# Kernel optimization log

Measured on AMD Instinct MI355X. Metric: run time of the kernel, lower is better.

The kernel has to match this reference:

```python
import jax, jax.numpy as jnp
import numpy as np

NUM_TYPES = 8
NUM_TAGS = 1 + 2 * NUM_TYPES  # tag 0 = 'O', 2t+1 = 'B-t', 2t+2 = 'I-t'
NEG = -10000.0


def _bio_constraints(num_types):
    K = 1 + 2 * num_types
    allowed = np.zeros((K, K), dtype=np.float32)
    for i in range(K):
        for j in range(K):
            if j == 0 or (j % 2 == 1):  # to O or to B-y: always allowed
                allowed[i, j] = 1.0
            else:  # to I-y: only from B-y or I-y
                y = (j - 2) // 2
                if i in (2 * y + 1, 2 * y + 2):
                    allowed[i, j] = 1.0
    start = np.array([1.0 if (j == 0 or j % 2 == 1) else 0.0 for j in range(K)], dtype=np.float32)
    end = np.ones((K,), dtype=np.float32)  # BIO: any tag may end a sequence
    return allowed, start, end


def setup_inputs() -> dict:
    key = jax.random.key(0)
    ks = jax.random.split(key, 8)
    B, T, D, K = 64, 512, 1024, NUM_TAGS
    mlm_out = jax.random.normal(ks[0], (B, T, D), dtype=jnp.float32)
    lengths = jax.random.randint(ks[1], (B,), T // 4, T + 1)  # variable lengths >= 1
    mask = (jnp.arange(T)[None, :] < lengths[:, None])  # bool [B,T], left-padded-free
    gold = jax.random.randint(ks[2], (B, T), 0, K)
    W = jax.random.normal(ks[3], (D, K), dtype=jnp.float32) * 0.02
    b = jnp.zeros((K,), dtype=jnp.float32)
    transitions = jax.random.normal(ks[4], (K, K), dtype=jnp.float32) * 0.1
    start_trans = jax.random.normal(ks[5], (K,), dtype=jnp.float32) * 0.1
    end_trans = jax.random.normal(ks[6], (K,), dtype=jnp.float32) * 0.1
    ta, sa, ea = _bio_constraints(NUM_TYPES)
    return {"mlm_out": mlm_out, "mask": mask, "gold": gold, "W": W, "b": b,
            "transitions": transitions, "start_trans": start_trans, "end_trans": end_trans,
            "trans_allowed": jnp.asarray(ta), "start_allowed": jnp.asarray(sa), "end_allowed": jnp.asarray(ea)}


def reference(mlm_out, mask, gold, W, b, transitions, start_trans, end_trans,
              trans_allowed, start_allowed, end_allowed):
    logits = jnp.einsum('btd,dk->btk', mlm_out, W) + b  # [B,T,K]
    maskf = mask.astype(logits.dtype)
    B, T, K = logits.shape

    # ---- joint (numerator) score, AllenNLP semantics ----
    score = start_trans[gold[:, 0]]
    pair = transitions[gold[:, :-1], gold[:, 1:]]                       # [B,T-1]
    emit = jnp.take_along_axis(logits, gold[:, :, None], axis=2)[..., 0]  # [B,T]
    score = score + jnp.sum(pair * maskf[:, 1:], axis=1) + jnp.sum(emit[:, :-1] * maskf[:, :-1], axis=1)
    lengths = jnp.sum(mask.astype(jnp.int32), axis=1)
    last_tags = jnp.take_along_axis(gold, (lengths - 1)[:, None], axis=1)[:, 0]
    last_emit = jnp.take_along_axis(logits[:, -1, :], last_tags[:, None], axis=1)[:, 0]
    score = score + end_trans[last_tags] + last_emit * maskf[:, -1]

    # ---- partition function (forward algorithm, log-space scan over time) ----
    logits_t = jnp.swapaxes(logits, 0, 1)  # [T,B,K]
    mask_t = jnp.swapaxes(maskf, 0, 1)     # [T,B]
    alpha0 = start_trans + logits_t[0]

    def fstep(alpha, xs):
        emit_t, m = xs
        inner = alpha[:, :, None] + transitions[None] + emit_t[:, None, :]  # [B,K,K]
        new = jax.scipy.special.logsumexp(inner, axis=1)
        return jnp.where(m[:, None] > 0, new, alpha), None

    alphaT, _ = jax.lax.scan(fstep, alpha0, (logits_t[1:], mask_t[1:]))
    logZ = jax.scipy.special.logsumexp(alphaT + end_trans, axis=1)

    loss = -jnp.sum(score - logZ)  # loss_weight = 1.0

    # ---- Viterbi decode with BIO-constrained transitions ----
    ct = transitions * trans_allowed + NEG * (1.0 - trans_allowed)
    cs = start_trans * start_allowed + NEG * (1.0 - start_allowed)
    ce = end_trans * end_allowed + NEG * (1.0 - end_allowed)
    v0 = cs + logits_t[0]

    def vstep(v, xs):
        emit_t, m = xs
        inner = v[:, :, None] + ct[None]          # [B,K,K]
        bp = jnp.argmax(inner, axis=1)            # [B,K] best prev tag per next tag
        best = jnp.max(inner, axis=1) + emit_t
        return jnp.where(m[:, None] > 0, best, v), bp

    vT, bps = jax.lax.scan(vstep, v0, (logits_t[1:], mask_t[1:]))  # bps [T-1,B,K]
    last_tag = jnp.argmax(vT + ce, axis=1)  # [B]

    def btstep(tag, xs):
        bp, m = xs
        prev = jnp.take_along_axis(bp, tag[:, None], axis=1)[:, 0]
        prev = jnp.where(m > 0, prev, tag)  # padded steps: carry tag through
        return prev, tag

    first_tag, tags_rest = jax.lax.scan(btstep, last_tag, (bps, mask_t[1:]), reverse=True)
    pred = jnp.concatenate([first_tag[None], tags_rest], axis=0).swapaxes(0, 1)  # [B,T]
    pred = pred * mask.astype(pred.dtype)
    return logits, loss, pred
```

## Files before the change

kernel.cpp:

```cpp
#include <hip/hip_runtime.h>
#include <math.h>

#define KK 17
#define TT 512
#define DD 1024
#define NBATCH 64
#define NEGC -10000.0f
#define NINF -1e30f

__device__ __forceinline__ float wsum64(float v) {
#pragma unroll
  for (int s = 32; s >= 1; s >>= 1) v += __shfl_xor(v, s);
  return v;
}
__device__ __forceinline__ float wmax64(float v) {
#pragma unroll
  for (int s = 32; s >= 1; s >>= 1) v = fmaxf(v, __shfl_xor(v, s));
  return v;
}
__device__ __forceinline__ int wsum64i(int v) {
#pragma unroll
  for (int s = 32; s >= 1; s >>= 1) v += __shfl_xor(v, s);
  return v;
}

__global__ __launch_bounds__(512) void k_logits(const float* __restrict__ X,
                                                const float* __restrict__ W,
                                                const float* __restrict__ b,
                                                float* __restrict__ logits) {
  __shared__ float Ws[512 * KK];
  const int tid = threadIdx.x;
  const int lane = tid & 63;
  const int wv = tid >> 6;
  const long r0 = (long)blockIdx.x * 16 + wv * 2;
  const float* x0 = X + r0 * DD;
  float a0[KK], a1[KK];
#pragma unroll
  for (int j = 0; j < KK; ++j) { a0[j] = 0.f; a1[j] = 0.f; }

  for (int half = 0; half < 2; ++half) {
    __syncthreads();
#pragma unroll
    for (int i = 0; i < KK; ++i) {
      int idx = tid + i * 512;
      Ws[idx] = W[half * 512 * KK + idx];
    }
    __syncthreads();
#pragma unroll
    for (int it = 0; it < 8; ++it) {
      int k = it * 64 + lane;
      float xa = x0[half * 512 + k];
      float xb = x0[DD + half * 512 + k];
#pragma unroll
      for (int j = 0; j < KK; ++j) {
        float w = Ws[k * KK + j];
        a0[j] = fmaf(xa, w, a0[j]);
        a1[j] = fmaf(xb, w, a1[j]);
      }
    }
  }
#pragma unroll
  for (int j = 0; j < KK; ++j) { a0[j] = wsum64(a0[j]); a1[j] = wsum64(a1[j]); }
  if (lane < KK) {
    float v0 = 0.f, v1 = 0.f;
#pragma unroll
    for (int j = 0; j < KK; ++j)
      if (lane == j) { v0 = a0[j]; v1 = a1[j]; }
    float bb = b[lane];
    logits[r0 * KK + lane] = v0 + bb;
    logits[(r0 + 1) * KK + lane] = v1 + bb;
  }
}

__global__ __launch_bounds__(128) void k_scan(
    const float* __restrict__ logits, const void* __restrict__ maskp,
    const int* __restrict__ gold, const float* __restrict__ trans,
    const float* __restrict__ st, const float* __restrict__ et,
    const float* __restrict__ ta, const float* __restrict__ sa,
    const float* __restrict__ ea, float* __restrict__ lossp,
    float* __restrict__ predp) {
  __shared__ __align__(16) float EM[513 * KK];
  __shared__ __align__(4) unsigned char Mk[512];
  __shared__ unsigned char BPt[511 * KK];
  __shared__ unsigned char G2t[256 * KK];
  __shared__ unsigned char G4t[128 * KK];
  __shared__ unsigned char G8t[64 * KK];
  __shared__ unsigned char PR[512];
  __shared__ float red[2];
  __shared__ int slen[2];
  __shared__ int shlt;

  const int tid = threadIdx.x;
  const int lane = tid & 63;
  const int wv = tid >> 6;
  const int batch = blockIdx.x & 63;
  const int role = blockIdx.x >> 6;
  const float* Lg = logits + (size_t)batch * TT * KK;

  const unsigned char* mb = (const unsigned char*)maskp;
  const bool m_is_i32 = (mb[1] == 0);

  {
    const float4* Lg4 = reinterpret_cast<const float4*>(Lg);
    float4* EM4 = reinterpret_cast<float4*>(EM);
    for (int i = tid; i < (TT * KK) / 4; i += 128) {
      float4 v = Lg4[i];
      if (role == 0) {
        v.x = expf(v.x); v.y = expf(v.y); v.z = expf(v.z); v.w = expf(v.w);
      }
      EM4[i] = v;
    }
    if (m_is_i32) {
      const int* mi = (const int*)maskp + batch * TT;
      for (int t2 = tid; t2 < TT; t2 += 128) Mk[t2] = (unsigned char)(mi[t2] != 0);
    } else {
      const unsigned char* mB = mb + batch * TT;
      for (int t2 = tid; t2 < TT; t2 += 128) Mk[t2] = (unsigned char)(mB[t2] != 0);
    }
  }
  __syncthreads();
  {
    unsigned int m4 = *reinterpret_cast<const unsigned int*>(&Mk[tid * 4]);
    int c = (int)((m4 * 0x01010101u) >> 24);
    c = wsum64i(c);
    if (lane == 0) slen[wv] = c;
  }
  __syncthreads();
  const int len = slen[0] + slen[1];

  if (role == 0) {
    if (wv == 0) {
      const int jc = lane < KK ? lane : (KK - 1);
      const bool act = lane < KK;
      float Pcol[KK];
#pragma unroll
      for (int i = 0; i < KK; ++i) Pcol[i] = expf(trans[i * KK + jc]);
      float a0 = st[jc] + Lg[jc];
      float m0 = wmax64(act ? a0 : NINF);
      float qown = expf(a0 - m0);
      float C = m0;
      float q[KK];
#pragma unroll
      for (int i = 0; i < KK; ++i) q[i] = __shfl(qown, i);
      float ee = EM[KK + jc];
      for (int t = 1; t < len; ++t) {
        float ee_n = EM[(t + 1) * KK + jc];
        float da = fmaf(q[0], Pcol[0], fmaf(q[4], Pcol[4], fmaf(q[8], Pcol[8], fmaf(q[12], Pcol[12], q[16] * Pcol[16]))));
        float db = fmaf(q[1], Pcol[1], fmaf(q[5], Pcol[5], fmaf(q[9], Pcol[9], q[13] * Pcol[13])));
        float dc = fmaf(q[2], Pcol[2], fmaf(q[6], Pcol[6], fmaf(q[10], Pcol[10], q[14] * Pcol[14])));
        float dd = fmaf(q[3], Pcol[3], fmaf(q[7], Pcol[7], fmaf(q[11], Pcol[11], q[15] * Pcol[15])));
        float qn = ((da + db) + (dc + dd)) * ee;
        ee = ee_n;
#pragma unroll
        for (int i = 0; i < KK; ++i) q[i] = __shfl(qn, i);
        qown = qn;
        if ((t & 7) == 0) {
          float s0 = ((q[0] + q[1]) + (q[2] + q[3])) + ((q[4] + q[5]) + (q[6] + q[7]));
          float s1 = ((q[8] + q[9]) + (q[10] + q[11])) + ((q[12] + q[13]) + (q[14] + q[15]));
          float s = (s0 + s1) + q[16];
          float inv = 1.0f / s;
          C += logf(s);
#pragma unroll
          for (int i = 0; i < KK; ++i) q[i] *= inv;
          qown *= inv;
        }
      }
      float term = act ? qown * expf(et[jc]) : 0.f;
      float S = wsum64(term);
      if (lane == 0) red[0] = C + logf(S);
    } else {
      const int* gb = gold + batch * TT;
      float esum = 0.f, tsum = 0.f;
#pragma unroll
      for (int u = 0; u < 8; ++u) {
        int t = lane + 64 * u;
        int gt = gb[t];
        float mt = (float)Mk[t];
        esum += mt * Lg[t * KK + gt];
        int tn = (t + 1 < TT) ? t + 1 : TT - 1;
        int gn = gb[tn];
        float mtr = (t + 1 < TT && Mk[t + 1]) ? 1.f : 0.f;
        tsum += mtr * trans[gt * KK + gn];
      }
      float ssum = wsum64(esum + tsum);
      if (lane == 0) red[1] = ssum + st[gb[0]] + et[gb[len - 1]];
    }
    __syncthreads();
    if (tid == 0) atomicAdd(lossp, red[0] - red[1]);
  } else {
    if (wv == 0) {
      const int jj = lane & 31;
      const int h = lane >> 5;
      const int jc = jj < KK ? jj : (KK - 1);
      const int i0 = h ? 9 : 0;
      const int ni = h ? 8 : 9;
      float ctv[9];
#pragma unroll
      for (int r = 0; r < 9; ++r) {
        int i = i0 + r;
        int ic = i < KK ? i : (KK - 1);
        float cv = (ta[ic * KK + jc] > 0.5f) ? trans[ic * KK + jc] : NEGC;
        ctv[r] = (r < ni) ? cv : NINF;
      }
      float v = ((sa[jc] > 0.5f) ? st[jc] : NEGC) + EM[jc];
      float ec = EM[KK + jc];
      for (int t = 1; t < len; ++t) {
        float en = EM[(t + 1) * KK + jc];
        float c0 = __shfl(v, i0 + 0) + ctv[0];
        float c1 = __shfl(v, i0 + 1) + ctv[1];
        float c2 = __shfl(v, i0 + 2) + ctv[2];
        float c3 = __shfl(v, i0 + 3) + ctv[3];
        float c4 = __shfl(v, i0 + 4) + ctv[4];
        float c5 = __shfl(v, i0 + 5) + ctv[5];
        float c6 = __shfl(v, i0 + 6) + ctv[6];
        float c7 = __shfl(v, i0 + 7) + ctv[7];
        float c8 = __shfl(v, i0 + 8) + ctv[8];
        float v01 = c1 > c0 ? c1 : c0; int i01 = c1 > c0 ? i0 + 1 : i0;
        float v23 = c3 > c2 ? c3 : c2; int i23 = c3 > c2 ? i0 + 3 : i0 + 2;
        float v45 = c5 > c4 ? c5 : c4; int i45 = c5 > c4 ? i0 + 5 : i0 + 4;
        float v67 = c7 > c6 ? c7 : c6; int i67 = c7 > c6 ? i0 + 7 : i0 + 6;
        float v03 = v23 > v01 ? v23 : v01; int i03 = v23 > v01 ? i23 : i01;
        float v47 = v67 > v45 ? v67 : v45; int i47 = v67 > v45 ? i67 : i45;
        float v07 = v47 > v03 ? v47 : v03; int i07 = v47 > v03 ? i47 : i03;
        float bv = c8 > v07 ? c8 : v07;   int bi = c8 > v07 ? i0 + 8 : i07;
        float ov = __shfl_xor(bv, 32);
        int oi = __shfl_xor(bi, 32);
        bool take = (ov > bv) || (ov == bv && oi < bi);
        bv = take ? ov : bv;
        bi = take ? oi : bi;
        BPt[(t - 1) * KK + jc] = (unsigned char)bi;
        v = bv + ec;
        ec = en;
      }
      float fv = (jj < KK) ? (v + ((ea[jc] > 0.5f) ? et[jc] : NEGC)) : NINF;
      int fi = jc;
#pragma unroll
      for (int s = 32; s >= 1; s >>= 1) {
        float ov = __shfl_xor(fv, s); int oi = __shfl_xor(fi, s);
        bool take = (ov > fv) || (ov == fv && oi < fi);
        fv = take ? ov : fv; fi = take ? oi : fi;
      }
      if (tid == 0) shlt = fi;
    }
    __syncthreads();
    const int lt = shlt;
    for (int m = tid; m < 256; m += 128) {
      int s1 = 2 * m + 1, s0 = 2 * m;
      bool u1 = (s1 < 511) && Mk[s1 + 1];
      bool u0 = Mk[s0 + 1] != 0;
#pragma unroll
      for (int x = 0; x < KK; ++x) {
        int y = u1 ? (int)BPt[s1 * KK + x] : x;
        int z = u0 ? (int)BPt[s0 * KK + y] : y;
        G2t[m * KK + x] = (unsigned char)z;
      }
    }
    __syncthreads();
    {
      int p = tid;
#pragma unroll
      for (int x = 0; x < KK; ++x) {
        int y = G2t[(2 * p + 1) * KK + x];
        G4t[p * KK + x] = G2t[2 * p * KK + y];
      }
    }
    __syncthreads();
    if (tid < 64) {
      int p = tid;
#pragma unroll
      for (int x = 0; x < KK; ++x) {
        int y = G4t[(2 * p + 1) * KK + x];
        G8t[p * KK + x] = G4t[2 * p * KK + y];
      }
    }
    __syncthreads();
    if (tid == 0) {
      int x = lt;
      for (int p = 63; p >= 0; --p) {
        x = G8t[p * KK + x];
        PR[8 * p] = (unsigned char)x;
      }
    }
    __syncthreads();
    if (tid < 64) {
      int p = tid;
      int src = (p == 63) ? lt : (int)PR[8 * p + 8];
      PR[8 * p + 4] = G4t[(2 * p + 1) * KK + src];
    }
    __syncthreads();
    {
      int m = tid;
      int src = (m == 127) ? lt : (int)PR[4 * m + 4];
      PR[4 * m + 2] = G2t[(2 * m + 1) * KK + src];
    }
    __syncthreads();
    for (int m = tid; m < 256; m += 128) {
      int s = 2 * m + 1;
      int src = (m == 255) ? lt : (int)PR[2 * m + 2];
      int val = ((s < 511) && Mk[s + 1]) ? (int)BPt[s * KK + src] : src;
      PR[2 * m + 1] = (unsigned char)val;
    }
    __syncthreads();
    float* po = predp + batch * TT;
    for (int t2 = tid; t2 < TT; t2 += 128) po[t2] = Mk[t2] ? (float)PR[t2] : 0.f;
  }
}

extern "C" void kernel_launch(void* const* d_in, const int* in_sizes, int n_in,
                              void* d_out, int out_size, void* d_ws, size_t ws_size,
                              hipStream_t stream) {
  const float* mlm = (const float*)d_in[0];
  const void* mask = d_in[1];
  const int* gold = (const int*)d_in[2];
  const float* W = (const float*)d_in[3];
  const float* b = (const float*)d_in[4];
  const float* trans = (const float*)d_in[5];
  const float* st = (const float*)d_in[6];
  const float* et = (const float*)d_in[7];
  const float* ta = (const float*)d_in[8];
  const float* sa = (const float*)d_in[9];
  const float* ea = (const float*)d_in[10];

  float* out = (float*)d_out;
  float* logits = out;
  float* lossp = out + (size_t)NBATCH * TT * KK;
  float* predp = lossp + 1;

  hipMemsetAsync(lossp, 0, sizeof(float), stream);
  k_logits<<<dim3(2048), dim3(512), 0, stream>>>(mlm, W, b, logits);
  k_scan<<<dim3(128), dim3(128), 0, stream>>>(logits, mask, gold, trans, st, et,
                                              ta, sa, ea, lossp, predp);
}
```

Before: 365.8 us.

## Merge forward and Viterbi scans into one block per batch using readlane broadcasts

The scan kernel now runs one 256-thread block per batch instead of two 128-thread blocks with separate roles. Viterbi, the forward algorithm and the gold score run concurrently on different wavefronts of the same block, sharing one load of the logits into LDS. Cross-lane shuffles are replaced with readlane broadcasts, and the Viterbi loop uses all 17 candidates per lane instead of splitting them across two half-waves. Exp is moved into the forward loop using fast __expf/__logf intrinsics, which changes numerical precision slightly.

New measurement: 368.3 us. No clear change (+0.7%).

```diff
diff --git a/kernel.cpp b/kernel.cpp
--- a/kernel.cpp
+++ b/kernel.cpp
@@ -13,15 +13,13 @@
   for (int s = 32; s >= 1; s >>= 1) v += __shfl_xor(v, s);
   return v;
 }
-__device__ __forceinline__ float wmax64(float v) {
-#pragma unroll
-  for (int s = 32; s >= 1; s >>= 1) v = fmaxf(v, __shfl_xor(v, s));
-  return v;
-}
 __device__ __forceinline__ int wsum64i(int v) {
 #pragma unroll
   for (int s = 32; s >= 1; s >>= 1) v += __shfl_xor(v, s);
   return v;
+}
+__device__ __forceinline__ float rl(float x, int i) {
+  return __int_as_float(__builtin_amdgcn_readlane(__float_as_int(x), i));
 }
 
 __global__ __launch_bounds__(512) void k_logits(const float* __restrict__ X,
@@ -72,7 +70,10 @@
   }
 }
 
-__global__ __launch_bounds__(128) void k_scan(
+#define ARGM(vl, il, vr, ir, vo, io) \
+  { bool tk = (vr) > (vl); vo = tk ? (vr) : (vl); io = tk ? (ir) : (il); }
+
+__global__ __launch_bounds__(256) void k_scan(
     const float* __restrict__ logits, const void* __restrict__ maskp,
     const int* __restrict__ gold, const float* __restrict__ trans,
     const float* __restrict__ st, const float* __restrict__ et,
@@ -87,14 +88,12 @@
   __shared__ unsigned char G8t[64 * KK];
   __shared__ unsigned char PR[512];
   __shared__ float red[2];
-  __shared__ int slen[2];
   __shared__ int shlt;
 
   const int tid = threadIdx.x;
   const int lane = tid & 63;
   const int wv = tid >> 6;
-  const int batch = blockIdx.x & 63;
-  const int role = blockIdx.x >> 6;
+  const int batch = blockIdx.x;
   const float* Lg = logits + (size_t)batch * TT * KK;
 
   const unsigned char* mb = (const unsigned char*)maskp;
@@ -103,207 +102,201 @@
   {
     const float4* Lg4 = reinterpret_cast<const float4*>(Lg);
     float4* EM4 = reinterpret_cast<float4*>(EM);
-    for (int i = tid; i < (TT * KK) / 4; i += 128) {
-      float4 v = Lg4[i];
-      if (role == 0) {
-        v.x = expf(v.x); v.y = expf(v.y); v.z = expf(v.z); v.w = expf(v.w);
-      }
-      EM4[i] = v;
-    }
+    for (int i = tid; i < (TT * KK) / 4; i += 256) EM4[i] = Lg4[i];
     if (m_is_i32) {
       const int* mi = (const int*)maskp + batch * TT;
-      for (int t2 = tid; t2 < TT; t2 += 128) Mk[t2] = (unsigned char)(mi[t2] != 0);
+      for (int t2 = tid; t2 < TT; t2 += 256) Mk[t2] = (unsigned char)(mi[t2] != 0);
     } else {
       const unsigned char* mB = mb + batch * TT;
-      for (int t2 = tid; t2 < TT; t2 += 128) Mk[t2] = (unsigned char)(mB[t2] != 0);
-    }
-  }
-  __syncthreads();
+      for (int t2 = tid; t2 < TT; t2 += 256) Mk[t2] = (unsigned char)(mB[t2] != 0);
+    }
+  }
+  __syncthreads();
+  int len;
   {
-    unsigned int m4 = *reinterpret_cast<const unsigned int*>(&Mk[tid * 4]);
-    int c = (int)((m4 * 0x01010101u) >> 24);
-    c = wsum64i(c);
-    if (lane == 0) slen[wv] = c;
-  }
-  __syncthreads();
-  const int len = slen[0] + slen[1];
-
-  if (role == 0) {
-    if (wv == 0) {
-      const int jc = lane < KK ? lane : (KK - 1);
-      const bool act = lane < KK;
-      float Pcol[KK];
-#pragma unroll
-      for (int i = 0; i < KK; ++i) Pcol[i] = expf(trans[i * KK + jc]);
-      float a0 = st[jc] + Lg[jc];
-      float m0 = wmax64(act ? a0 : NINF);
-      float qown = expf(a0 - m0);
-      float C = m0;
-      float q[KK];
-#pragma unroll
-      for (int i = 0; i < KK; ++i) q[i] = __shfl(qown, i);
-      float ee = EM[KK + jc];
-      for (int t = 1; t < len; ++t) {
-        float ee_n = EM[(t + 1) * KK + jc];
-        float da = fmaf(q[0], Pcol[0], fmaf(q[4], Pcol[4], fmaf(q[8], Pcol[8], fmaf(q[12], Pcol[12], q[16] * Pcol[16]))));
-        float db = fmaf(q[1], Pcol[1], fmaf(q[5], Pcol[5], fmaf(q[9], Pcol[9], q[13] * Pcol[13])));
-        float dc = fmaf(q[2], Pcol[2], fmaf(q[6], Pcol[6], fmaf(q[10], Pcol[10], q[14] * Pcol[14])));
-        float dd = fmaf(q[3], Pcol[3], fmaf(q[7], Pcol[7], fmaf(q[11], Pcol[11], q[15] * Pcol[15])));
-        float qn = ((da + db) + (dc + dd)) * ee;
-        ee = ee_n;
-#pragma unroll
-        for (int i = 0; i < KK; ++i) q[i] = __shfl(qn, i);
-        qown = qn;
-        if ((t & 7) == 0) {
-          float s0 = ((q[0] + q[1]) + (q[2] + q[3])) + ((q[4] + q[5]) + (q[6] + q[7]));
-          float s1 = ((q[8] + q[9]) + (q[10] + q[11])) + ((q[12] + q[13]) + (q[14] + q[15]));
-          float s = (s0 + s1) + q[16];
-          float inv = 1.0f / s;
-          C += logf(s);
-#pragma unroll
-          for (int i = 0; i < KK; ++i) q[i] *= inv;
-          qown *= inv;
-        }
+    const unsigned int* Mku = reinterpret_cast<const unsigned int*>(Mk);
+    unsigned int a = Mku[lane], b2 = Mku[64 + lane];
+    int c = (int)(((a * 0x01010101u) >> 24) + ((b2 * 0x01010101u) >> 24));
+    len = wsum64i(c);
+  }
+
+  const int jc = lane < KK ? lane : (KK - 1);
+
+  if (wv == 0) {
+    float ctv[KK];
+#pragma unroll
+    for (int i = 0; i < KK; ++i)
+      ctv[i] = (ta[i * KK + jc] > 0.5f) ? trans[i * KK + jc] : NEGC;
+    float v = ((sa[jc] > 0.5f) ? st[jc] : NEGC) + EM[jc];
+    float ec = EM[KK + jc];
+    const float* EMp = EM + 2 * KK + jc;
+    unsigned char* bpw = BPt + jc;
+    const bool act = lane < KK;
+    for (int t = 1; t < len; ++t) {
+      float en = *EMp;
+      EMp += KK;
+      float c0 = rl(v, 0) + ctv[0],  c1 = rl(v, 1) + ctv[1];
+      float c2 = rl(v, 2) + ctv[2],  c3 = rl(v, 3) + ctv[3];
+      float c4 = rl(v, 4) + ctv[4],  c5 = rl(v, 5) + ctv[5];
+      float c6 = rl(v, 6) + ctv[6],  c7 = rl(v, 7) + ctv[7];
+      float c8 = rl(v, 8) + ctv[8],  c9 = rl(v, 9) + ctv[9];
+      float c10 = rl(v, 10) + ctv[10], c11 = rl(v, 11) + ctv[11];
+      float c12 = rl(v, 12) + ctv[12], c13 = rl(v, 13) + ctv[13];
+      float c14 = rl(v, 14) + ctv[14], c15 = rl(v, 15) + ctv[15];
+      float c16 = rl(v, 16) + ctv[16];
+      float d0, d1, d2, d3, d4, d5, d6, d7;
+      int j0, j1, j2, j3, j4, j5, j6, j7;
+      ARGM(c0, 0, c1, 1, d0, j0)     ARGM(c2, 2, c3, 3, d1, j1)
+      ARGM(c4, 4, c5, 5, d2, j2)     ARGM(c6, 6, c7, 7, d3, j3)
+      ARGM(c8, 8, c9, 9, d4, j4)     ARGM(c10, 10, c11, 11, d5, j5)
+      ARGM(c12, 12, c13, 13, d6, j6) ARGM(c14, 14, c15, 15, d7, j7)
+      float e0, e1, e2, e3; int k0, k1, k2, k3;
+      ARGM(d0, j0, d1, j1, e0, k0)   ARGM(d2, j2, d3, j3, e1, k1)
+      ARGM(d4, j4, d5, j5, e2, k2)   ARGM(d6, j6, d7, j7, e3, k3)
+      float f0, f1; int l0, l1;
+      ARGM(e0, k0, e1, k1, f0, l0)   ARGM(e2, k2, e3, k3, f1, l1)
+      float g0; int m0i;
+      ARGM(f0, l0, f1, l1, g0, m0i)
+      float bv; int bi;
+      ARGM(g0, m0i, c16, 16, bv, bi)
+      if (act) bpw[0] = (unsigned char)bi;
+      bpw += KK;
+      v = bv + ec;
+      ec = en;
+    }
+    float fv = v + ((ea[jc] > 0.5f) ? et[jc] : NEGC);
+    float best = rl(fv, 0);
+    int bidx = 0;
+#pragma unroll
+    for (int i = 1; i < KK; ++i) {
+      float fi = rl(fv, i);
+      bool tk = fi > best;
+      best = tk ? fi : best;
+      bidx = tk ? i : bidx;
+    }
+    if (tid == 0) shlt = bidx;
+  } else if (wv == 1) {
+    float Pcol[KK];
+#pragma unroll
+    for (int i = 0; i < KK; ++i) Pcol[i] = __expf(trans[i * KK + jc]);
+    float a0 = st[jc] + EM[jc];
+    float m0 = rl(a0, 0);
+#pragma unroll
+    for (int i = 1; i < KK; ++i) m0 = fmaxf(m0, rl(a0, i));
+    float qown = __expf(a0 - m0);
+    float C = m0;
+    float ee = __expf(EM[KK + jc]);
+    const float* EMp = EM + 2 * KK + jc;
+    for (int t = 1; t < len; ++t) {
+      float en_raw = *EMp;
+      EMp += KK;
+      float q0 = rl(qown, 0), q1 = rl(qown, 1), q2 = rl(qown, 2), q3 = rl(qown, 3);
+      float q4 = rl(qown, 4), q5 = rl(qown, 5), q6 = rl(qown, 6), q7 = rl(qown, 7);
+      float q8 = rl(qown, 8), q9 = rl(qown, 9), q10 = rl(qown, 10), q11 = rl(qown, 11);
+      float q12 = rl(qown, 12), q13 = rl(qown, 13), q14 = rl(qown, 14), q15 = rl(qown, 15);
+      float q16 = rl(qown, 16);
+      float da = fmaf(q0, Pcol[0], fmaf(q4, Pcol[4], fmaf(q8, Pcol[8], fmaf(q12, Pcol[12], q16 * Pcol[16]))));
+      float db = fmaf(q1, Pcol[1], fmaf(q5, Pcol[5], fmaf(q9, Pcol[9], q13 * Pcol[13])));
+      float dc = fmaf(q2, Pcol[2], fmaf(q6, Pcol[6], fmaf(q10, Pcol[10], q14 * Pcol[14])));
+      float dd = fmaf(q3, Pcol[3], fmaf(q7, Pcol[7], fmaf(q11, Pcol[11], q15 * Pcol[15])));
+      float qn = ((da + db) + (dc + dd)) * ee;
+      ee = __expf(en_raw);
+      if ((t & 7) == 0) {
+        float s0 = ((q0 + q1) + (q2 + q3)) + ((q4 + q5) + (q6 + q7));
+        float s1 = ((q8 + q9) + (q10 + q11)) + ((q12 + q13) + (q14 + q15));
+        float s = (s0 + s1) + q16;
+        C += __logf(s);
+        qn *= (1.0f / s);
       }
-      float term = act ? qown * expf(et[jc]) : 0.f;
-      float S = wsum64(term);
-      if (lane == 0) red[0] = C + logf(S);
-    } else {
-      const int* gb = gold + batch * TT;
-      float esum = 0.f, tsum = 0.f;
-#pragma unroll
-      for (int u = 0; u < 8; ++u) {
-        int t = lane + 64 * u;
-        int gt = gb[t];
-        float mt = (float)Mk[t];
-        esum += mt * Lg[t * KK + gt];
-        int tn = (t + 1 < TT) ? t + 1 : TT - 1;
-        int gn = gb[tn];
-        float mtr = (t + 1 < TT && Mk[t + 1]) ? 1.f : 0.f;
-        tsum += mtr * trans[gt * KK + gn];
-      }
-      float ssum = wsum64(esum + tsum);
-      if (lane == 0) red[1] = ssum + st[gb[0]] + et[gb[len - 1]];
-    }
-    __syncthreads();
-    if (tid == 0) atomicAdd(lossp, red[0] - red[1]);
-  } else {
-    if (wv == 0) {
-      const int jj = lane & 31;
-      const int h = lane >> 5;
-      const int jc = jj < KK ? jj : (KK - 1);
-      const int i0 = h ? 9 : 0;
-      const int ni = h ? 8 : 9;
-      float ctv[9];
-#pragma unroll
-      for (int r = 0; r < 9; ++r) {
-        int i = i0 + r;
-        int ic = i < KK ? i : (KK - 1);
-        float cv = (ta[ic * KK + jc] > 0.5f) ? trans[ic * KK + jc] : NEGC;
-        ctv[r] = (r < ni) ? cv : NINF;
-      }
-      float v = ((sa[jc] > 0.5f) ? st[jc] : NEGC) + EM[jc];
-      float ec = EM[KK + jc];
-      for (int t = 1; t < len; ++t) {
-        float en = EM[(t + 1) * KK + jc];
-        float c0 = __shfl(v, i0 + 0) + ctv[0];
-        float c1 = __shfl(v, i0 + 1) + ctv[1];
-        float c2 = __shfl(v, i0 + 2) + ctv[2];
-        float c3 = __shfl(v, i0 + 3) + ctv[3];
-        float c4 = __shfl(v, i0 + 4) + ctv[4];
-        float c5 = __shfl(v, i0 + 5) + ctv[5];
-        float c6 = __shfl(v, i0 + 6) + ctv[6];
-        float c7 = __shfl(v, i0 + 7) + ctv[7];
-        float c8 = __shfl(v, i0 + 8) + ctv[8];
-        float v01 = c1 > c0 ? c1 : c0; int i01 = c1 > c0 ? i0 + 1 : i0;
-        float v23 = c3 > c2 ? c3 : c2; int i23 = c3 > c2 ? i0 + 3 : i0 + 2;
-        float v45 = c5 > c4 ? c5 : c4; int i45 = c5 > c4 ? i0 + 5 : i0 + 4;
-        float v67 = c7 > c6 ? c7 : c6; int i67 = c7 > c6 ? i0 + 7 : i0 + 6;
-        float v03 = v23 > v01 ? v23 : v01; int i03 = v23 > v01 ? i23 : i01;
-        float v47 = v67 > v45 ? v67 : v45; int i47 = v67 > v45 ? i67 : i45;
-        float v07 = v47 > v03 ? v47 : v03; int i07 = v47 > v03 ? i47 : i03;
-        float bv = c8 > v07 ? c8 : v07;   int bi = c8 > v07 ? i0 + 8 : i07;
-        float ov = __shfl_xor(bv, 32);
-        int oi = __shfl_xor(bi, 32);
-        bool take = (ov > bv) || (ov == bv && oi < bi);
-        bv = take ? ov : bv;
-        bi = take ? oi : bi;
-        BPt[(t - 1) * KK + jc] = (unsigned char)bi;
-        v = bv + ec;
-        ec = en;
-      }
-      float fv = (jj < KK) ? (v + ((ea[jc] > 0.5f) ? et[jc] : NEGC)) : NINF;
-      int fi = jc;
-#pragma unroll
-      for (int s = 32; s >= 1; s >>= 1) {
-        float ov = __shfl_xor(fv, s); int oi = __shfl_xor(fi, s);
-        bool take = (ov > fv) || (ov == fv && oi < fi);
-        fv = take ? ov : fv; fi = take ? oi : fi;
-      }
-      if (tid == 0) shlt = fi;
-    }
-    __syncthreads();
-    const int lt = shlt;
-    for (int m = tid; m < 256; m += 128) {
-      int s1 = 2 * m + 1, s0 = 2 * m;
-      bool u1 = (s1 < 511) && Mk[s1 + 1];
-      bool u0 = Mk[s0 + 1] != 0;
-#pragma unroll
-      for (int x = 0; x < KK; ++x) {
-        int y = u1 ? (int)BPt[s1 * KK + x] : x;
-        int z = u0 ? (int)BPt[s0 * KK + y] : y;
-        G2t[m * KK + x] = (unsigned char)z;
-      }
-    }
-    __syncthreads();
-    {
-      int p = tid;
-#pragma unroll
-      for (int x = 0; x < KK; ++x) {
-        int y = G2t[(2 * p + 1) * KK + x];
-        G4t[p * KK + x] = G2t[2 * p * KK + y];
-      }
-    }
-    __syncthreads();
-    if (tid < 64) {
-      int p = tid;
-#pragma unroll
-      for (int x = 0; x < KK; ++x) {
-        int y = G4t[(2 * p + 1) * KK + x];
-        G8t[p * KK + x] = G4t[2 * p * KK + y];
-      }
-    }
-    __syncthreads();
-    if (tid == 0) {
-      int x = lt;
-      for (int p = 63; p >= 0; --p) {
-        x = G8t[p * KK + x];
-        PR[8 * p] = (unsigned char)x;
-      }
-    }
-    __syncthreads();
-    if (tid < 64) {
-      int p = tid;
-      int src = (p == 63) ? lt : (int)PR[8 * p + 8];
-      PR[8 * p + 4] = G4t[(2 * p + 1) * KK + src];
-    }
-    __syncthreads();
-    {
-      int m = tid;
-      int src = (m == 127) ? lt : (int)PR[4 * m + 4];
-      PR[4 * m + 2] = G2t[(2 * m + 1) * KK + src];
-    }
-    __syncthreads();
-    for (int m = tid; m < 256; m += 128) {
-      int s = 2 * m + 1;
-      int src = (m == 255) ? lt : (int)PR[2 * m + 2];
-      int val = ((s < 511) && Mk[s + 1]) ? (int)BPt[s * KK + src] : src;
-      PR[2 * m + 1] = (unsigned char)val;
-    }
-    __syncthreads();
-    float* po = predp + batch * TT;
-    for (int t2 = tid; t2 < TT; t2 += 128) po[t2] = Mk[t2] ? (float)PR[t2] : 0.f;
-  }
+      qown = qn;
+    }
+    float term = qown * __expf(et[jc]);
+    float S = rl(term, 0);
+#pragma unroll
+    for (int i = 1; i < KK; ++i) S += rl(term, i);
+    if (lane == 0) red[0] = C + __logf(S);
+  } else if (wv == 2) {
+    const int* gb = gold + batch * TT;
+    float esum = 0.f, tsum = 0.f;
+#pragma unroll
+    for (int u = 0; u < 8; ++u) {
+      int t = lane + 64 * u;
+      int gt = gb[t];
+      float mt = (float)Mk[t];
+      esum += mt * EM[t * KK + gt];
+      int tn = (t + 1 < TT) ? t + 1 : TT - 1;
+      int gn = gb[tn];
+      float mtr = (t + 1 < TT && Mk[t + 1]) ? 1.f : 0.f;
+      tsum += mtr * trans[gt * KK + gn];
+    }
+    float ssum = wsum64(esum + tsum);
+    if (lane == 0) red[1] = ssum + st[gb[0]] + et[gb[len - 1]];
+  }
+  __syncthreads();
+  if (tid == 0) atomicAdd(lossp, red[0] - red[1]);
+
+  const int lt = shlt;
+  {
+    int m = tid;
+    int s1 = 2 * m + 1, s0b = 2 * m;
+    bool u1 = (s1 < 511) && Mk[s1 + 1];
+    bool u0 = Mk[s0b + 1] != 0;
+#pragma unroll
+    for (int x = 0; x < KK; ++x) {
+      int y = u1 ? (int)BPt[s1 * KK + x] : x;
+      int z = u0 ? (int)BPt[s0b * KK + y] : y;
+      G2t[m * KK + x] = (unsigned char)z;
+    }
+  }
+  __syncthreads();
+  if (tid < 128) {
+    int p = tid;
+#pragma unroll
+    for (int x = 0; x < KK; ++x) {
+      int y = G2t[(2 * p + 1) * KK + x];
+      G4t[p * KK + x] = G2t[2 * p * KK + y];
+    }
+  }
+  __syncthreads();
+  if (tid < 64) {
+    int p = tid;
+#pragma unroll
+    for (int x = 0; x < KK; ++x) {
+      int y = G4t[(2 * p + 1) * KK + x];
+      G8t[p * KK + x] = G4t[2 * p * KK + y];
+    }
+  }
+  __syncthreads();
+  if (tid == 0) {
+    int x = lt;
+    for (int p = 63; p >= 0; --p) {
+      x = G8t[p * KK + x];
+      PR[8 * p] = (unsigned char)x;
+    }
+  }
+  __syncthreads();
+  if (tid < 64) {
+    int p = tid;
+    int src = (p == 63) ? lt : (int)PR[8 * p + 8];
+    PR[8 * p + 4] = G4t[(2 * p + 1) * KK + src];
+  }
+  __syncthreads();
+  if (tid < 128) {
+    int m = tid;
+    int src = (m == 127) ? lt : (int)PR[4 * m + 4];
+    PR[4 * m + 2] = G2t[(2 * m + 1) * KK + src];
+  }
+  __syncthreads();
+  {
+    int m = tid;
+    int s = 2 * m + 1;
+    int src = (m == 255) ? lt : (int)PR[2 * m + 2];
+    int val = ((s < 511) && Mk[s + 1]) ? (int)BPt[s * KK + src] : src;
+    PR[2 * m + 1] = (unsigned char)val;
+  }
+  __syncthreads();
+  float* po = predp + batch * TT;
+  for (int t2 = tid; t2 < TT; t2 += 256) po[t2] = Mk[t2] ? (float)PR[t2] : 0.f;
 }
 
 extern "C" void kernel_launch(void* const* d_in, const int* in_sizes, int n_in,
@@ -328,6 +321,6 @@
 
   hipMemsetAsync(lossp, 0, sizeof(float), stream);
   k_logits<<<dim3(2048), dim3(512), 0, stream>>>(mlm, W, b, logits);
-  k_scan<<<dim3(128), dim3(128), 0, stream>>>(logits, mask, gold, trans, st, et,
-                                              ta, sa, ea, lossp, predp);
-}
+  k_scan<<<dim3(64), dim3(256), 0, stream>>>(logits, mask, gold, trans, st, et,
+                                             ta, sa, ea, lossp, predp);
+}
```
